# Optimization experiments

Hardware: AMD Instinct MI355X
Metric: run time of the kernel (lower is better)

Reference implementation:

```python
import jax, jax.numpy as jnp
import numpy as np

TT_SHAPE = (8, 8, 12, 8, 8)   # prod = 49152 = 768*64
RANK = 5


def tt_to_matrix(cores, in_dim, out_dim):
    """Contract TT cores [1,n0,r],[r,n1,r],...,[r,n4,1] into a dense [in_dim, out_dim] matrix."""
    t = cores[0]                      # [1, n0, r]
    for c in cores[1:]:
        t = jnp.tensordot(t, c, axes=([-1], [0]))   # grows mode dims, keeps trailing rank
    t = jnp.squeeze(t, axis=(0, -1))  # [n0,n1,n2,n3,n4]
    return t.reshape(in_dim, out_dim)


def setup_inputs() -> dict:
    key = jax.random.key(0)
    ks = jax.random.split(key, 13)
    ranks = [1, RANK, RANK, RANK, RANK, 1]
    scale = 0.3  # keep reconstructed weight in a sane init range

    def make_cores(keys):
        return [scale * jax.random.normal(keys[i], (ranks[i], TT_SHAPE[i], ranks[i + 1]), dtype=jnp.float32)
                for i in range(5)]

    down_cores = make_cores(ks[0:5])
    up_cores = make_cores(ks[5:10])
    inputs = {
        'hidden_states': jax.random.normal(ks[10], (16, 2048, 768), dtype=jnp.float32),
        'b_down': jnp.zeros((64,), dtype=jnp.float32),
        'b_up': jnp.zeros((768,), dtype=jnp.float32),
    }
    for i in range(5):
        inputs[f'd{i}'] = down_cores[i]
        inputs[f'u{i}'] = up_cores[i]
    return inputs


def reference(hidden_states, d0, d1, d2, d3, d4, u0, u1, u2, u3, u4, b_down, b_up):
    # down projection: TT-decomposed Linear(768 -> 64)
    W_down = tt_to_matrix([d0, d1, d2, d3, d4], 768, 64)   # in=8*8*12, out=8*8
    # up projection: TT-decomposed Linear(64 -> 768)
    W_up = tt_to_matrix([u0, u1, u2, u3, u4], 64, 768)     # in=8*8, out=12*8*8
    down = jnp.einsum('bsh,ha->bsa', hidden_states, W_down) + b_down
    act = jax.nn.gelu(down, approximate=False)             # HF ACT2FN['gelu'] is exact erf gelu
    up = jnp.einsum('bsa,ah->bsh', act, W_up) + b_up
    return hidden_states + up
```

## Files before the change

kernel.cpp:

```cpp
#include <hip/hip_runtime.h>


typedef __attribute__((ext_vector_type(8))) short bf16x8;
typedef __attribute__((ext_vector_type(4))) float f32x4;

__device__ __forceinline__ unsigned short f2bf(float f) {
    union { float f; unsigned u; } v; v.f = f;
    unsigned r = (v.u + 0x7FFFu + ((v.u >> 16) & 1u)) >> 16;
    return (unsigned short)r;
}

__device__ __forceinline__ float tt_entry(
    const float* c0, const float* c1, const float* c2,
    const float* c3, const float* c4,
    int i0, int i1, int i2, int i3, int i4)
{
    float v1[5], v2[5], v3[5];
#pragma unroll
    for (int r2 = 0; r2 < 5; ++r2) {
        float s = 0.f;
#pragma unroll
        for (int r1 = 0; r1 < 5; ++r1)
            s += c0[i0 * 5 + r1] * c1[(r1 * 8 + i1) * 5 + r2];
        v1[r2] = s;
    }
#pragma unroll
    for (int r3 = 0; r3 < 5; ++r3) {
        float s = 0.f;
#pragma unroll
        for (int r2 = 0; r2 < 5; ++r2)
            s += v1[r2] * c2[(r2 * 12 + i2) * 5 + r3];
        v2[r3] = s;
    }
#pragma unroll
    for (int r4 = 0; r4 < 5; ++r4) {
        float s = 0.f;
#pragma unroll
        for (int r3 = 0; r3 < 5; ++r3)
            s += v2[r3] * c3[(r3 * 8 + i3) * 5 + r4];
        v3[r4] = s;
    }
    float w = 0.f;
#pragma unroll
    for (int r4 = 0; r4 < 5; ++r4)
        w += v3[r4] * c4[r4 * 8 + i4];
    return w;
}

__global__ __launch_bounds__(256) void tt_build_frags(
    const float* __restrict__ d0, const float* __restrict__ d1,
    const float* __restrict__ d2, const float* __restrict__ d3,
    const float* __restrict__ d4,
    const float* __restrict__ u0, const float* __restrict__ u1,
    const float* __restrict__ u2, const float* __restrict__ u3,
    const float* __restrict__ u4,
    unsigned short* __restrict__ wdFrag, unsigned short* __restrict__ wuFrag)
{
    __shared__ float cs[1560];
    {
        const float* srcs[10] = { d0, d1, d2, d3, d4, u0, u1, u2, u3, u4 };
        const int sizes[10]   = { 40, 200, 300, 200, 40, 40, 200, 300, 200, 40 };
        const int offs[10]    = { 0, 40, 240, 540, 740, 780, 820, 1020, 1320, 1520 };
#pragma unroll
        for (int c = 0; c < 10; ++c)
            for (int i = threadIdx.x; i < sizes[c]; i += 256)
                cs[offs[c] + i] = srcs[c][i];
    }
    __syncthreads();

    int e = blockIdx.x * 256 + threadIdx.x;
    bool isUp = (e >= 49152);
    int idx = isUp ? (e - 49152) : e;
    int j    = idx & 7;
    int lane = (idx >> 3) & 63;
    int tile = idx >> 9;
    int kg = lane >> 4, ln = lane & 15;

    if (!isUp) {
        int ks = tile >> 2, nt = tile & 3;
        int k = ks * 32 + kg * 8 + j;
        int a = nt * 16 + ln;
        int i0 = k / 96, i1 = (k / 12) % 8, i2 = k % 12;
        int i3 = a >> 3, i4 = a & 7;
        float w = tt_entry(cs + 0, cs + 40, cs + 240, cs + 540, cs + 740,
                           i0, i1, i2, i3, i4);
        wdFrag[idx] = f2bf(w);
    } else {
        int s = tile / 48, ht = tile % 48;
        int aIn = s * 32 + kg * 8 + j;
        int h = ht * 16 + ln;
        int i0 = aIn >> 3, i1 = aIn & 7;
        int i2 = h / 64, i3 = (h >> 3) & 7, i4 = h & 7;
        float w = tt_entry(cs + 780, cs + 820, cs + 1020, cs + 1320, cs + 1520,
                           i0, i1, i2, i3, i4);
        wuFrag[idx] = f2bf(w);
    }
}

#define MT 16

__global__ __launch_bounds__(256) void adapter_fused(
    const float* __restrict__ hs,
    const float* __restrict__ b_down,
    const float* __restrict__ b_up,
    const unsigned short* __restrict__ wdFrag,
    const unsigned short* __restrict__ wuFrag,
    float* __restrict__ out)
{
    __shared__ float hs_s[MT * 768];
    __shared__ unsigned short act_s[MT * 64];

    const int t    = threadIdx.x;
    const int lane = t & 63;
    const int w    = t >> 6;
    const int ln   = lane & 15;
    const int kg   = lane >> 4;

    const int row0 = blockIdx.x * MT;

    {
        const char* gbase = (const char*)(hs + (size_t)row0 * 768);
#pragma unroll
        for (int i = 0; i < 12; ++i) {
            unsigned d = (unsigned)(i * 4096 + w * 1024 + lane * 16);
            unsigned row = d / 3072u;
            unsigned src = d ^ ((row & 7u) << 4);
            __builtin_amdgcn_global_load_lds(
                (const __attribute__((address_space(1))) unsigned int*)(gbase + src),
                (__attribute__((address_space(3))) unsigned int*)
                    ((char*)hs_s + i * 4096 + w * 1024),
                16, 0, 0);
        }
    }
    __syncthreads();

    const unsigned swzA = (unsigned)((ln & 7) << 4);
    f32x4 acc1 = (f32x4){0.f, 0.f, 0.f, 0.f};

#pragma unroll 8
    for (int ks = 0; ks < 24; ++ks) {
        unsigned a0 = ((unsigned)(ln * 3072 + ks * 128 + kg * 32)) ^ swzA;
        f32x4 fa = *(const f32x4*)((const char*)hs_s + a0);
        f32x4 fb = *(const f32x4*)((const char*)hs_s + (a0 ^ 16u));
        bf16x8 afrag;
        afrag[0] = (short)f2bf(fa[0]); afrag[1] = (short)f2bf(fa[1]);
        afrag[2] = (short)f2bf(fa[2]); afrag[3] = (short)f2bf(fa[3]);
        afrag[4] = (short)f2bf(fb[0]); afrag[5] = (short)f2bf(fb[1]);
        afrag[6] = (short)f2bf(fb[2]); afrag[7] = (short)f2bf(fb[3]);
        bf16x8 bfrag = *(const bf16x8*)(wdFrag + (((ks * 4 + w) * 64) + lane) * 8);
        acc1 = __builtin_amdgcn_mfma_f32_16x16x32_bf16(afrag, bfrag, acc1, 0, 0, 0);
    }

    {
        const int a = w * 16 + ln;
        const float bd = b_down[a];
#pragma unroll
        for (int r = 0; r < 4; ++r) {
            const int rr = kg * 4 + r;
            float x = acc1[r] + bd;
            float g = 0.5f * x * (1.0f + erff(x * 0.70710678118654752f));
            unsigned off = ((unsigned)(rr * 128 + a * 2)) ^ ((unsigned)((rr & 7) << 4));
            *(unsigned short*)((char*)act_s + off) = f2bf(g);
        }
    }
    __syncthreads();

    bf16x8 pa[2];
    {
        const unsigned swz = (unsigned)((ln & 7) << 4);
#pragma unroll
        for (int s = 0; s < 2; ++s) {
            unsigned off = ((unsigned)(ln * 128 + s * 64 + kg * 16)) ^ swz;
            pa[s] = *(const bf16x8*)((const char*)act_s + off);
        }
    }

#pragma unroll 4
    for (int n2 = 0; n2 < 12; ++n2) {
        const int ht = w * 12 + n2;
        f32x4 acc = (f32x4){0.f, 0.f, 0.f, 0.f};
#pragma unroll
        for (int s = 0; s < 2; ++s) {
            bf16x8 bfrag = *(const bf16x8*)(wuFrag + (((s * 48 + ht) * 64) + lane) * 8);
            acc = __builtin_amdgcn_mfma_f32_16x16x32_bf16(pa[s], bfrag, acc, 0, 0, 0);
        }
        const int h = ht * 16 + ln;
        const float bu = b_up[h];
#pragma unroll
        for (int r = 0; r < 4; ++r) {
            const int rr = kg * 4 + r;
            unsigned off = ((unsigned)(rr * 3072 + h * 4)) ^ ((unsigned)((rr & 7) << 4));
            float hv = *(const float*)((const char*)hs_s + off);
            out[(size_t)(row0 + rr) * 768 + h] = acc[r] + hv + bu;
        }
    }
}

extern "C" void kernel_launch(void* const* d_in, const int* in_sizes, int n_in,
                              void* d_out, int out_size, void* d_ws, size_t ws_size,
                              hipStream_t stream) {
    const float* hs = (const float*)d_in[0];
    const float* bd = (const float*)d_in[1];
    const float* bu = (const float*)d_in[2];
    const float* d0 = (const float*)d_in[3];
    const float* u0 = (const float*)d_in[4];
    const float* d1 = (const float*)d_in[5];
    const float* u1 = (const float*)d_in[6];
    const float* d2 = (const float*)d_in[7];
    const float* u2 = (const float*)d_in[8];
    const float* d3 = (const float*)d_in[9];
    const float* u3 = (const float*)d_in[10];
    const float* d4 = (const float*)d_in[11];
    const float* u4 = (const float*)d_in[12];

    unsigned short* wdFrag = (unsigned short*)d_ws;
    unsigned short* wuFrag = wdFrag + 49152;

    tt_build_frags<<<384, 256, 0, stream>>>(d0, d1, d2, d3, d4,
                                            u0, u1, u2, u3, u4,
                                            wdFrag, wuFrag);

    const int rows = 16 * 2048;
    adapter_fused<<<rows / MT, 256, 0, stream>>>(hs, bd, bu, wdFrag, wuFrag,
                                                 (float*)d_out);
}
```

Measured before the change: 48.83 us.

## Give each wave its own 16-row tile, drop block-wide LDS staging and barriers

```diff
diff --git a/kernel.cpp b/kernel.cpp
--- a/kernel.cpp
+++ b/kernel.cpp
@@ -1,4 +1,5 @@
 #include <hip/hip_runtime.h>
+#include <hip/hip_bf16.h>
 
 
 typedef __attribute__((ext_vector_type(8))) short bf16x8;
@@ -97,9 +98,17 @@
     }
 }
 
-#define MT 16
-
-__global__ __launch_bounds__(256) void adapter_fused(
+
+__device__ __forceinline__ bf16x8 cvt8(f32x4 a, f32x4 b) {
+    union { bf16x8 v; __hip_bfloat162 h[4]; } r;
+    r.h[0] = __float22bfloat162_rn(make_float2(a[0], a[1]));
+    r.h[1] = __float22bfloat162_rn(make_float2(a[2], a[3]));
+    r.h[2] = __float22bfloat162_rn(make_float2(b[0], b[1]));
+    r.h[3] = __float22bfloat162_rn(make_float2(b[2], b[3]));
+    return r.v;
+}
+
+__global__ __launch_bounds__(256, 2) void adapter_fused(
     const float* __restrict__ hs,
     const float* __restrict__ b_down,
     const float* __restrict__ b_up,
@@ -107,92 +116,82 @@
     const unsigned short* __restrict__ wuFrag,
     float* __restrict__ out)
 {
-    __shared__ float hs_s[MT * 768];
-    __shared__ unsigned short act_s[MT * 64];
+    __shared__ char lds[4][4608];
 
     const int t    = threadIdx.x;
     const int lane = t & 63;
     const int w    = t >> 6;
     const int ln   = lane & 15;
     const int kg   = lane >> 4;
-
-    const int row0 = blockIdx.x * MT;
-
-    {
-        const char* gbase = (const char*)(hs + (size_t)row0 * 768);
-#pragma unroll
-        for (int i = 0; i < 12; ++i) {
-            unsigned d = (unsigned)(i * 4096 + w * 1024 + lane * 16);
-            unsigned row = d / 3072u;
-            unsigned src = d ^ ((row & 7u) << 4);
-            __builtin_amdgcn_global_load_lds(
-                (const __attribute__((address_space(1))) unsigned int*)(gbase + src),
-                (__attribute__((address_space(3))) unsigned int*)
-                    ((char*)hs_s + i * 4096 + w * 1024),
-                16, 0, 0);
-        }
-    }
-    __syncthreads();
-
-    const unsigned swzA = (unsigned)((ln & 7) << 4);
-    f32x4 acc1 = (f32x4){0.f, 0.f, 0.f, 0.f};
+    char* myl = lds[w];
+
+    const int wrow0 = blockIdx.x * 64 + w * 16;
+    const float* hsrow = hs + (size_t)(wrow0 + ln) * 768;
+
+    f32x4 acc[4];
+#pragma unroll
+    for (int nt = 0; nt < 4; ++nt) acc[nt] = (f32x4){0.f, 0.f, 0.f, 0.f};
 
 #pragma unroll 8
     for (int ks = 0; ks < 24; ++ks) {
-        unsigned a0 = ((unsigned)(ln * 3072 + ks * 128 + kg * 32)) ^ swzA;
-        f32x4 fa = *(const f32x4*)((const char*)hs_s + a0);
-        f32x4 fb = *(const f32x4*)((const char*)hs_s + (a0 ^ 16u));
-        bf16x8 afrag;
-        afrag[0] = (short)f2bf(fa[0]); afrag[1] = (short)f2bf(fa[1]);
-        afrag[2] = (short)f2bf(fa[2]); afrag[3] = (short)f2bf(fa[3]);
-        afrag[4] = (short)f2bf(fb[0]); afrag[5] = (short)f2bf(fb[1]);
-        afrag[6] = (short)f2bf(fb[2]); afrag[7] = (short)f2bf(fb[3]);
-        bf16x8 bfrag = *(const bf16x8*)(wdFrag + (((ks * 4 + w) * 64) + lane) * 8);
-        acc1 = __builtin_amdgcn_mfma_f32_16x16x32_bf16(afrag, bfrag, acc1, 0, 0, 0);
-    }
-
-    {
-        const int a = w * 16 + ln;
-        const float bd = b_down[a];
+        f32x4 fa = *(const f32x4*)(hsrow + ks * 32 + kg * 8);
+        f32x4 fb = *(const f32x4*)(hsrow + ks * 32 + kg * 8 + 4);
+        bf16x8 afrag = cvt8(fa, fb);
+#pragma unroll
+        for (int nt = 0; nt < 4; ++nt) {
+            bf16x8 bfrag = *(const bf16x8*)(wdFrag + (((ks * 4 + nt) * 64) + lane) * 8);
+            acc[nt] = __builtin_amdgcn_mfma_f32_16x16x32_bf16(afrag, bfrag, acc[nt], 0, 0, 0);
+        }
+    }
+
+#pragma unroll
+    for (int nt = 0; nt < 4; ++nt) {
+        const float bd = b_down[nt * 16 + ln];
 #pragma unroll
         for (int r = 0; r < 4; ++r) {
             const int rr = kg * 4 + r;
-            float x = acc1[r] + bd;
+            float x = acc[nt][r] + bd;
             float g = 0.5f * x * (1.0f + erff(x * 0.70710678118654752f));
-            unsigned off = ((unsigned)(rr * 128 + a * 2)) ^ ((unsigned)((rr & 7) << 4));
-            *(unsigned short*)((char*)act_s + off) = f2bf(g);
+            unsigned off = ((unsigned)(rr * 128 + (nt * 16 + ln) * 2))
+                         ^ ((unsigned)((rr & 7) << 4));
+            *(__hip_bfloat16*)(myl + off) = __float2bfloat16(g);
         }
     }
-    __syncthreads();
+    asm volatile("s_waitcnt lgkmcnt(0)" ::: "memory");
 
     bf16x8 pa[2];
-    {
-        const unsigned swz = (unsigned)((ln & 7) << 4);
+#pragma unroll
+    for (int s = 0; s < 2; ++s) {
+        unsigned off = ((unsigned)(ln * 128 + s * 64 + kg * 16))
+                     ^ ((unsigned)((ln & 7) << 4));
+        pa[s] = *(const bf16x8*)(myl + off);
+    }
+
+    char* tbuf = myl + 2048;
+    const int trow = lane >> 2;
+    const int tc   = (lane & 3) * 4;
+
+#pragma unroll 4
+    for (int n2 = 0; n2 < 48; ++n2) {
+        char* tb = tbuf + (n2 & 1) * 1280;
+        f32x4 a2 = (f32x4){0.f, 0.f, 0.f, 0.f};
 #pragma unroll
         for (int s = 0; s < 2; ++s) {
-            unsigned off = ((unsigned)(ln * 128 + s * 64 + kg * 16)) ^ swz;
-            pa[s] = *(const bf16x8*)((const char*)act_s + off);
+            bf16x8 bfrag = *(const bf16x8*)(wuFrag + (((s * 48 + n2) * 64) + lane) * 8);
+            a2 = __builtin_amdgcn_mfma_f32_16x16x32_bf16(pa[s], bfrag, a2, 0, 0, 0);
         }
-    }
-
-#pragma unroll 4
-    for (int n2 = 0; n2 < 12; ++n2) {
-        const int ht = w * 12 + n2;
-        f32x4 acc = (f32x4){0.f, 0.f, 0.f, 0.f};
-#pragma unroll
-        for (int s = 0; s < 2; ++s) {
-            bf16x8 bfrag = *(const bf16x8*)(wuFrag + (((s * 48 + ht) * 64) + lane) * 8);
-            acc = __builtin_amdgcn_mfma_f32_16x16x32_bf16(pa[s], bfrag, acc, 0, 0, 0);
-        }
-        const int h = ht * 16 + ln;
-        const float bu = b_up[h];
-#pragma unroll
-        for (int r = 0; r < 4; ++r) {
-            const int rr = kg * 4 + r;
-            unsigned off = ((unsigned)(rr * 3072 + h * 4)) ^ ((unsigned)((rr & 7) << 4));
-            float hv = *(const float*)((const char*)hs_s + off);
-            out[(size_t)(row0 + rr) * 768 + h] = acc[r] + hv + bu;
-        }
+#pragma unroll
+        for (int r = 0; r < 4; ++r)
+            *(float*)(tb + (kg * 4 + r) * 80 + ln * 4) = a2[r];
+        asm volatile("s_waitcnt lgkmcnt(0)" ::: "memory");
+        f32x4 tv = *(const f32x4*)(tb + trow * 80 + tc * 4);
+        size_t goff = (size_t)(wrow0 + trow) * 768 + n2 * 16 + tc;
+        f32x4 hv = *(const f32x4*)(hs + goff);
+        f32x4 bu = *(const f32x4*)(b_up + n2 * 16 + tc);
+        f32x4 o;
+#pragma unroll
+        for (int j = 0; j < 4; ++j) o[j] = tv[j] + hv[j] + bu[j];
+        *(f32x4*)(out + goff) = o;
     }
 }
 
@@ -221,6 +220,6 @@
                                             wdFrag, wuFrag);
 
     const int rows = 16 * 2048;
-    adapter_fused<<<rows / MT, 256, 0, stream>>>(hs, bd, bu, wdFrag, wuFrag,
+    adapter_fused<<<rows / 64, 256, 0, stream>>>(hs, bd, bu, wdFrag, wuFrag,
                                                  (float*)d_out);
 }
```

Result: slower. 76.34 us (+56.3%).
